# Performance work log

Hardware: AMD Instinct MI355X
Metric: run time of the kernel (lower is better)

## Reference

```python
import jax, jax.numpy as jnp
import numpy as np

B, N, M, C1, C2, H = 16, 4096, 1024, 256, 512, 256
SE_C = max(1, int(H / 24.0))  # 10
BN_EPS = 1e-5

def _bn(x, g, b):
    # training-mode BatchNorm over (B, n) per channel; x: [B, C, n]
    mean = jnp.mean(x, axis=(0, 2), keepdims=True)
    var = jnp.mean((x - mean) ** 2, axis=(0, 2), keepdims=True)  # biased var (torch)
    return (x - mean) * jax.lax.rsqrt(var + BN_EPS) * g[None, :, None] + b[None, :, None]

def _swish(x):
    return x * jax.nn.sigmoid(x)

def setup_inputs() -> dict:
    key = jax.random.key(0)
    ks = jax.random.split(key, 12)
    d = {
        "unknown": jax.random.normal(ks[0], (B, N, 3), jnp.float32),
        "known": jax.random.normal(ks[1], (B, M, 3), jnp.float32),
        "unknow_feats": jax.random.normal(ks[2], (B, C1, N), jnp.float32),
        "known_feats": jax.random.normal(ks[3], (B, C2, M), jnp.float32),
        # conv1 (C1+C2 -> H), no bias (bn)
        "W1": jax.random.normal(ks[4], (H, C1 + C2), jnp.float32) * (1.0 / np.sqrt(C1 + C2)),
        "g1": jnp.ones((H,), jnp.float32),
        "b1": jnp.zeros((H,), jnp.float32),
        # SE block (1x1 convs with bias, no pooling in this impl)
        "se_rw": jax.random.normal(ks[5], (SE_C, H), jnp.float32) * (1.0 / np.sqrt(H)),
        "se_rb": jnp.zeros((SE_C,), jnp.float32),
        "se_ew": jax.random.normal(ks[6], (H, SE_C), jnp.float32) * (1.0 / np.sqrt(SE_C)),
        "se_eb": jnp.zeros((H,), jnp.float32),
        # conv2 (H -> H), no bias
        "W2": jax.random.normal(ks[7], (H, H), jnp.float32) * (1.0 / np.sqrt(H)),
        "g2": jnp.ones((H,), jnp.float32),
        "b2": jnp.zeros((H,), jnp.float32),
    }
    return d

def reference(unknown, known, unknow_feats, known_feats,
              W1, g1, b1, se_rw, se_rb, se_ew, se_eb, W2, g2, b2):
    # three_nn: squared distances of each unknown point to all known points
    d2 = jnp.sum((unknown[:, :, None, :] - known[:, None, :, :]) ** 2, axis=-1)  # [B,N,M]
    neg_d, idx = jax.lax.top_k(-d2, 3)  # 3 smallest
    dist = -neg_d                                       # [B,N,3]
    dist_recip = 1.0 / (dist + 1e-8)
    weight = dist_recip / jnp.sum(dist_recip, axis=2, keepdims=True)  # [B,N,3]
    # three_interpolate: gather known_feats at idx, inverse-distance weighted sum
    gathered = jnp.take_along_axis(known_feats[:, :, None, :], idx[:, None, :, :], axis=3)  # [B,C2,N,3]
    interp = jnp.sum(gathered * weight[:, None, :, :], axis=-1)  # [B,C2,N]
    x = jnp.concatenate([interp, unknow_feats], axis=1)  # [B,C1+C2,N]
    # conv1 (1x1) + BN + SE
    h = jnp.einsum('oc,bcn->bon', W1, x)
    h = _bn(h, g1, b1)
    s = jnp.einsum('oc,bcn->bon', se_rw, h) + se_rb[None, :, None]
    s = _swish(s)
    s = jnp.einsum('oc,bcn->bon', se_ew, s) + se_eb[None, :, None]
    h = jax.nn.sigmoid(s) * h
    # conv2 (1x1) + BN + ReLU
    h = jnp.einsum('oc,bcn->bon', W2, h)
    h = _bn(h, g2, b2)
    return jax.nn.relu(h)  # [B, H, N]
```

## Files before the change

kernel.cpp:

```cpp
#include <hip/hip_runtime.h>
#include <math.h>

#define B_ 16
#define N_ 4096
#define M_ 1024
#define C1_ 256
#define C2_ 512
#define H_ 256
#define SEC_ 10
#define OC_ 8
#define BN_EPS 1e-5f

typedef _Float16 f16;
typedef f16 f16x8 __attribute__((ext_vector_type(8)));
typedef f16 f16x4 __attribute__((ext_vector_type(4)));
typedef f16 f16x2 __attribute__((ext_vector_type(2)));
typedef float f32x4 __attribute__((ext_vector_type(4)));

__global__ __launch_bounds__(256)
void three_nn_kernel(const float* __restrict__ unknown, const float* __restrict__ known,
                     int* __restrict__ idxp, float* __restrict__ wgtp)
{
    __shared__ float kx[M_], ky[M_], kz[M_];
    __shared__ float cd[4][64][3];
    __shared__ int   ci[4][64][3];
    const int b  = blockIdx.y;
    const int bn = blockIdx.x * 64;
    const int t  = threadIdx.x;
    const float* kb = known + (long)b * M_ * 3;

    {
        const float4 q0 = *(const float4*)(kb + 12*t);
        const float4 q1 = *(const float4*)(kb + 12*t + 4);
        const float4 q2 = *(const float4*)(kb + 12*t + 8);
        const int m = 4*t;
        kx[m+0]=q0.x; ky[m+0]=q0.y; kz[m+0]=q0.z;
        kx[m+1]=q0.w; ky[m+1]=q1.x; kz[m+1]=q1.y;
        kx[m+2]=q1.z; ky[m+2]=q1.w; kz[m+2]=q2.x;
        kx[m+3]=q2.y; ky[m+3]=q2.z; kz[m+3]=q2.w;
    }
    __syncthreads();

    const int w = t >> 6, ln = t & 63;
    const int n = bn + ln;
    const float* up = unknown + ((long)b * N_ + n) * 3;
    const float ux = up[0], uy = up[1], uz = up[2];

    float b0 = 1e30f, b1v = 1e30f, b2v = 1e30f;
    int j0 = 0, j1 = 0, j2 = 0;

    const int m0 = w * 256;
    for (int m = m0; m < m0 + 256; m += 4) {
        const float4 X = *(const float4*)&kx[m];
        const float4 Y = *(const float4*)&ky[m];
        const float4 Z = *(const float4*)&kz[m];
        const float px[4] = {X.x, X.y, X.z, X.w};
        const float py[4] = {Y.x, Y.y, Y.z, Y.w};
        const float pz[4] = {Z.x, Z.y, Z.z, Z.w};
        #pragma unroll
        for (int q = 0; q < 4; q++) {
            const float dx = ux - px[q], dy = uy - py[q], dz = uz - pz[q];
            const float d = dx*dx + dy*dy + dz*dz;
            if (d < b2v) {
                const int mm = m + q;
                if (d < b1v) {
                    b2v = b1v; j2 = j1;
                    if (d < b0) { b1v = b0; j1 = j0; b0 = d; j0 = mm; }
                    else        { b1v = d;  j1 = mm; }
                } else { b2v = d; j2 = mm; }
            }
        }
    }
    cd[w][ln][0] = b0;  cd[w][ln][1] = b1v; cd[w][ln][2] = b2v;
    ci[w][ln][0] = j0;  ci[w][ln][1] = j1;  ci[w][ln][2] = j2;
    __syncthreads();

    if (t < 64) {
        float d0 = cd[0][t][0], d1 = cd[0][t][1], d2 = cd[0][t][2];
        int   i0 = ci[0][t][0], i1 = ci[0][t][1], i2 = ci[0][t][2];
        #pragma unroll
        for (int c = 1; c < 4; c++) {
            #pragma unroll
            for (int j = 0; j < 3; j++) {
                const float d = cd[c][t][j];
                const int  ix = ci[c][t][j];
                if (d < d2) {
                    if (d < d1) {
                        d2 = d1; i2 = i1;
                        if (d < d0) { d1 = d0; i1 = i0; d0 = d; i0 = ix; }
                        else        { d1 = d;  i1 = ix; }
                    } else { d2 = d; i2 = ix; }
                }
            }
        }
        const float r0 = 1.f/(d0 + 1e-8f), r1 = 1.f/(d1 + 1e-8f), r2 = 1.f/(d2 + 1e-8f);
        const float rs = 1.f/(r0 + r1 + r2);
        const long base = ((long)b * N_ + bn + t) * 3;
        idxp[base+0] = i0; idxp[base+1] = i1; idxp[base+2] = i2;
        wgtp[base+0] = r0*rs; wgtp[base+1] = r1*rs; wgtp[base+2] = r2*rs;
    }
}

template<int MODE>
__global__ __launch_bounds__(256)
void gemm_mfma(const float* __restrict__ A, int lda,
               const float* __restrict__ Bf, const f16* __restrict__ Bh,
               long strideB, int ldb, int K,
               f16* __restrict__ Ch, long strideC, int ldc,
               const f16* __restrict__ Gt,
               const int* __restrict__ idxp, const float* __restrict__ wgtp,
               float* __restrict__ psum,
               const float* __restrict__ spart, const float* __restrict__ rbAdj,
               const float* __restrict__ se_ewp, const float* __restrict__ se_ebp,
               const float* __restrict__ a1p, const float* __restrict__ c1p)
{
    __shared__ __align__(16) f16 As[256*72];
    __shared__ __align__(16) f16 Bs[64*72];
    __shared__ float sswl[SEC_*64];

    const int b   = blockIdx.z;
    const int bn  = blockIdx.x * 64;
    const int tid = threadIdx.x;
    const int l = tid & 63, w = tid >> 6;
    const int lane16 = l & 15, quad = l >> 4;

    const float* Bfb = nullptr;
    const f16*   Bhb = nullptr;
    if constexpr (MODE == 2) Bhb = Bh + (long)b*strideB;
    else                     Bfb = Bf + (long)b*strideB;

    if constexpr (MODE == 2) {
        for (int i = tid; i < SEC_*64; i += 256) {
            const int j = i >> 6, nn = i & 63;
            float v = rbAdj[j];
            #pragma unroll
            for (int oc = 0; oc < OC_; oc++)
                v += spart[(((long)oc*B_ + b)*SEC_ + j)*N_ + bn + nn];
            sswl[j*64 + nn] = v / (1.f + __expf(-v));
        }
        __syncthreads();
    }

    f32x4 acc[4][4];
    #pragma unroll
    for (int i = 0; i < 4; i++)
        #pragma unroll
        for (int j = 0; j < 4; j++)
            acc[i][j] = (f32x4){0.f, 0.f, 0.f, 0.f};

    const int akb = (tid & 3) * 16;
    const int arw = tid >> 2;

    for (int k0 = 0; k0 < K; k0 += 64) {
        #pragma unroll
        for (int p = 0; p < 4; p++) {
            const int r = p*64 + arw;
            const float* src = A + (long)r*lda + k0 + akb;
            const float4 v0 = *(const float4*)(src);
            const float4 v1 = *(const float4*)(src + 4);
            const float4 v2 = *(const float4*)(src + 8);
            const float4 v3 = *(const float4*)(src + 12);
            f16x8 h0, h1;
            h0[0]=(f16)v0.x; h0[1]=(f16)v0.y; h0[2]=(f16)v0.z; h0[3]=(f16)v0.w;
            h0[4]=(f16)v1.x; h0[5]=(f16)v1.y; h0[6]=(f16)v1.z; h0[7]=(f16)v1.w;
            h1[0]=(f16)v2.x; h1[1]=(f16)v2.y; h1[2]=(f16)v2.z; h1[3]=(f16)v2.w;
            h1[4]=(f16)v3.x; h1[5]=(f16)v3.y; h1[6]=(f16)v3.z; h1[7]=(f16)v3.w;
            *(f16x8*)&As[r*72 + akb]     = h0;
            *(f16x8*)&As[r*72 + akb + 8] = h1;
        }
        #pragma unroll
        for (int it = 0; it < 2; it++) {
            const int slot = it*256 + tid;
            const int k2 = slot >> 4;
            const int n0 = (slot & 15) * 4;
            if constexpr (MODE == 2) {
                const int ka = k0 + 2*k2;
                const f16* s0 = Bhb + (long)ka*ldb + bn + n0;
                const f16x4 ua = *(const f16x4*)s0;
                const f16x4 ub = *(const f16x4*)(s0 + ldb);
                float val[2][4];
                #pragma unroll
                for (int r = 0; r < 2; r++) {
                    const int kr = ka + r;
                    const float aa = a1p[kr], cc = c1p[kr], eb = se_ebp[kr];
                    const float* ew = se_ewp + kr*SEC_;
                    #pragma unroll
                    for (int j = 0; j < 4; j++) {
                        float e = eb;
                        #pragma unroll
                        for (int q = 0; q < SEC_; q++) e += ew[q]*sswl[q*64 + n0 + j];
                        const float g  = 1.f/(1.f + __expf(-e));
                        const float hv = (r == 0) ? (float)ua[j] : (float)ub[j];
                        val[r][j] = g * (aa*hv + cc);
                    }
                }
                #pragma unroll
                for (int j = 0; j < 4; j++) {
                    f16x2 p; p[0] = (f16)val[0][j]; p[1] = (f16)val[1][j];
                    *(f16x2*)&Bs[(n0+j)*72 + 2*k2] = p;
                }
            } else {
                const float* s0 = Bfb + (long)(k0 + 2*k2)*ldb + bn + n0;
                const float4 u = *(const float4*)s0;
                const float4 v = *(const float4*)(s0 + ldb);
                f16x2 p0, p1, p2, p3;
                p0[0]=(f16)u.x; p0[1]=(f16)v.x;
                p1[0]=(f16)u.y; p1[1]=(f16)v.y;
                p2[0]=(f16)u.z; p2[1]=(f16)v.z;
                p3[0]=(f16)u.w; p3[1]=(f16)v.w;
                *(f16x2*)&Bs[(n0+0)*72 + 2*k2] = p0;
                *(f16x2*)&Bs[(n0+1)*72 + 2*k2] = p1;
                *(f16x2*)&Bs[(n0+2)*72 + 2*k2] = p2;
                *(f16x2*)&Bs[(n0+3)*72 + 2*k2] = p3;
            }
        }
        __syncthreads();
        const int abase = (w*64 + lane16)*72 + quad*8;
        const int bbase = lane16*72 + quad*8;
        #pragma unroll
        for (int s = 0; s < 2; s++) {
            f16x8 af[4], bf[4];
            #pragma unroll
            for (int i = 0; i < 4; i++) af[i] = *(const f16x8*)&As[abase + i*1152 + s*32];
            #pragma unroll
            for (int j = 0; j < 4; j++) bf[j] = *(const f16x8*)&Bs[bbase + j*1152 + s*32];
            #pragma unroll
            for (int i = 0; i < 4; i++)
                #pragma unroll
                for (int j = 0; j < 4; j++)
                    acc[i][j] = __builtin_amdgcn_mfma_f32_16x16x32_f16(af[i], bf[j], acc[i][j], 0, 0, 0);
        }
        __syncthreads();
    }

    if constexpr (MODE == 0) {
        f16* Gl = As;
        #pragma unroll
        for (int i = 0; i < 4; i++)
            #pragma unroll
            for (int r = 0; r < 4; r++) {
                const int h = w*64 + i*16 + quad*4 + r;
                #pragma unroll
                for (int j = 0; j < 4; j++)
                    Gl[(j*16 + lane16)*264 + h] = (f16)acc[i][j][r];
            }
        __syncthreads();
        f16* Gtb = Ch + (long)b*strideC + (long)bn*H_;
        #pragma unroll
        for (int it = 0; it < 8; it++) {
            const int t = it*256 + tid;
            const int m = t >> 5, c = (t & 31)*8;
            *(f16x8*)&Gtb[m*H_ + c] = *(const f16x8*)&Gl[m*264 + c];
        }
    } else {
        if constexpr (MODE == 1) {
            f16* P = As;
            const int p  = tid >> 2;
            const int qd = tid & 3;
            const long ib = ((long)b*N_ + bn + p)*3;
            const int i0 = idxp[ib], i1 = idxp[ib+1], i2 = idxp[ib+2];
            const float w0 = wgtp[ib], w1 = wgtp[ib+1], w2 = wgtp[ib+2];
            const f16* gb = Gt + (long)b*M_*H_;
            const f16* g0 = gb + (long)i0*H_ + qd*64;
            const f16* g1 = gb + (long)i1*H_ + qd*64;
            const f16* g2 = gb + (long)i2*H_ + qd*64;
            f16* Pr = P + p*264 + qd*64;
            #pragma unroll
            for (int c = 0; c < 64; c += 8) {
                const f16x8 x0 = *(const f16x8*)&g0[c];
                const f16x8 x1 = *(const f16x8*)&g1[c];
                const f16x8 x2 = *(const f16x8*)&g2[c];
                f16x8 o;
                #pragma unroll
                for (int e = 0; e < 8; e++)
                    o[e] = (f16)(w0*(float)x0[e] + w1*(float)x1[e] + w2*(float)x2[e]);
                *(f16x8*)&Pr[c] = o;
            }
            __syncthreads();
            #pragma unroll
            for (int i = 0; i < 4; i++)
                #pragma unroll
                for (int r = 0; r < 4; r++) {
                    const int h = w*64 + i*16 + quad*4 + r;
                    #pragma unroll
                    for (int j = 0; j < 4; j++)
                        acc[i][j][r] += (float)P[(j*16 + lane16)*264 + h];
                }
        }
        const int bid = blockIdx.z * gridDim.x + blockIdx.x;
        float* ps = psum + (long)bid * (2*H_);
        f16* Cb = Ch + (long)b*strideC;
        #pragma unroll
        for (int i = 0; i < 4; i++)
            #pragma unroll
            for (int r = 0; r < 4; r++) {
                const int row = w*64 + i*16 + quad*4 + r;
                float s1 = 0.f, s2 = 0.f;
                #pragma unroll
                for (int j = 0; j < 4; j++) {
                    const float v = acc[i][j][r];
                    s1 += v; s2 += v*v;
                    Cb[(long)row*ldc + bn + j*16 + lane16] = (f16)v;
                }
                #pragma unroll
                for (int off = 1; off < 16; off <<= 1) {
                    s1 += __shfl_xor(s1, off, 64);
                    s2 += __shfl_xor(s2, off, 64);
                }
                if (lane16 == 0) {
                    ps[row]      = s1;
                    ps[H_ + row] = s2;
                }
            }
    }
}

__global__ __launch_bounds__(256)
void reduce_stats_kernel(const float* __restrict__ psum, float* __restrict__ stats, int nblk)
{
    __shared__ float red[8][33];
    const int o  = blockIdx.x*32 + (threadIdx.x & 31);
    const int ch = threadIdx.x >> 5;
    float s = 0.f;
    for (int bid = ch; bid < nblk; bid += 8)
        s += psum[(long)bid*(2*H_) + o];
    red[ch][threadIdx.x & 31] = s;
    __syncthreads();
    if (ch == 0) {
        float t = 0.f;
        #pragma unroll
        for (int c = 0; c < 8; c++) t += red[c][threadIdx.x & 31];
        stats[o] = t;
    }
}

__global__ __launch_bounds__(256)
void finalize1_kernel(const float* __restrict__ stats,
                      const float* __restrict__ g, const float* __restrict__ bb,
                      const float* __restrict__ se_rw, const float* __restrict__ se_rb,
                      float* __restrict__ a1, float* __restrict__ c1,
                      float* __restrict__ rw2, float* __restrict__ rbAdj)
{
    __shared__ float cbuf[H_];
    __shared__ float red[256];
    const int o = threadIdx.x;
    const float inv = 1.f / (float)(B_ * N_);
    const float S1 = stats[o], S2 = stats[H_ + o];
    const float mean = S1 * inv;
    const float var  = S2 * inv - mean*mean;
    const float a = g[o] * rsqrtf(var + BN_EPS);
    const float c = bb[o] - mean*a;
    a1[o] = a; c1[o] = c; cbuf[o] = c;
    for (int j = 0; j < SEC_; j++) rw2[j*H_ + o] = se_rw[j*H_ + o] * a;
    __syncthreads();
    for (int j = 0; j < SEC_; j++) {
        red[o] = se_rw[j*H_ + o] * cbuf[o];
        __syncthreads();
        for (int s = 128; s > 0; s >>= 1) {
            if (o < s) red[o] += red[o + s];
            __syncthreads();
        }
        if (o == 0) rbAdj[j] = se_rb[j] + red[0];
        __syncthreads();
    }
}

__global__ __launch_bounds__(256)
void se_reduce_kernel(const f16* __restrict__ h1h, const float* __restrict__ rw2,
                      float* __restrict__ spart)
{
    constexpr int OCH = H_ / OC_;
    __shared__ float rwl[SEC_][OCH];
    const int b = blockIdx.y, oc = blockIdx.z;
    const int n0 = blockIdx.x*1024 + threadIdx.x*4;
    for (int i = threadIdx.x; i < SEC_*OCH; i += 256)
        rwl[i/OCH][i%OCH] = rw2[(i/OCH)*H_ + oc*OCH + (i%OCH)];
    __syncthreads();
    f32x4 acc[SEC_];
    #pragma unroll
    for (int j = 0; j < SEC_; j++) acc[j] = (f32x4){0.f,0.f,0.f,0.f};
    const f16* hp = h1h + ((long)b*H_ + oc*OCH)*N_ + n0;
    for (int o = 0; o < OCH; o++) {
        const f16x4 h = *(const f16x4*)(hp + (long)o*N_);
        f32x4 hf; hf[0]=(float)h[0]; hf[1]=(float)h[1]; hf[2]=(float)h[2]; hf[3]=(float)h[3];
        #pragma unroll
        for (int j = 0; j < SEC_; j++) acc[j] += rwl[j][o]*hf;
    }
    #pragma unroll
    for (int j = 0; j < SEC_; j++)
        *(f32x4*)&spart[(((long)oc*B_ + b)*SEC_ + j)*N_ + n0] = acc[j];
}

__global__ __launch_bounds__(256)
void finalize2_kernel(const float* __restrict__ stats,
                      const float* __restrict__ g, const float* __restrict__ bb,
                      float* __restrict__ a2, float* __restrict__ c2)
{
    const int o = threadIdx.x;
    const float inv = 1.f / (float)(B_ * N_);
    const float S1 = stats[o], S2 = stats[H_ + o];
    const float mean = S1 * inv;
    const float var  = S2 * inv - mean*mean;
    const float a = g[o] * rsqrtf(var + BN_EPS);
    a2[o] = a; c2[o] = bb[o] - mean*a;
}

__global__ __launch_bounds__(256)
void bn_relu_kernel(const f16* __restrict__ h2h, float* __restrict__ out,
                    const float* __restrict__ a2, const float* __restrict__ c2)
{
    const long e = ((long)blockIdx.x*256 + threadIdx.x)*8;
    const int o = (int)((e >> 12) & (H_ - 1));
    const f16x8 v = *(const f16x8*)(h2h + e);
    const float a = a2[o], c = c2[o];
    float4 r0, r1;
    r0.x = fmaxf(a*(float)v[0] + c, 0.f);
    r0.y = fmaxf(a*(float)v[1] + c, 0.f);
    r0.z = fmaxf(a*(float)v[2] + c, 0.f);
    r0.w = fmaxf(a*(float)v[3] + c, 0.f);
    r1.x = fmaxf(a*(float)v[4] + c, 0.f);
    r1.y = fmaxf(a*(float)v[5] + c, 0.f);
    r1.z = fmaxf(a*(float)v[6] + c, 0.f);
    r1.w = fmaxf(a*(float)v[7] + c, 0.f);
    *(float4*)(out + e)     = r0;
    *(float4*)(out + e + 4) = r1;
}

extern "C" void kernel_launch(void* const* d_in, const int* in_sizes, int n_in,
                              void* d_out, int out_size, void* d_ws, size_t ws_size,
                              hipStream_t stream)
{
    const float* unknown = (const float*)d_in[0];
    const float* known   = (const float*)d_in[1];
    const float* uf      = (const float*)d_in[2];
    const float* kf      = (const float*)d_in[3];
    const float* W1      = (const float*)d_in[4];
    const float* g1      = (const float*)d_in[5];
    const float* b1      = (const float*)d_in[6];
    const float* se_rw   = (const float*)d_in[7];
    const float* se_rb   = (const float*)d_in[8];
    const float* se_ew   = (const float*)d_in[9];
    const float* se_eb   = (const float*)d_in[10];
    const float* W2      = (const float*)d_in[11];
    const float* g2      = (const float*)d_in[12];
    const float* b2      = (const float*)d_in[13];

    char* ws = (char*)d_ws;
    size_t off = 0;
    auto alloc = [&](size_t bytes) -> void* {
        void* p = ws + off;
        off += (bytes + 255) & ~(size_t)255;
        return p;
    };
    const int NBLK = (N_/64) * B_;
    int*   idxp   = (int*)  alloc((size_t)B_*N_*3*4);
    float* wgtp   = (float*)alloc((size_t)B_*N_*3*4);
    f16*   Gt     = (f16*)  alloc((size_t)B_*M_*H_*2);
    f16*   h1h    = (f16*)  alloc((size_t)B_*H_*N_*2);
    f16*   h2h    = (f16*)  alloc((size_t)B_*H_*N_*2);
    float* spart  = (float*)alloc((size_t)OC_*B_*SEC_*N_*4);
    float* psum1  = (float*)alloc((size_t)NBLK*2*H_*4);
    float* psum2  = (float*)alloc((size_t)NBLK*2*H_*4);
    float* stats1 = (float*)alloc(2*H_*4);
    float* stats2 = (float*)alloc(2*H_*4);
    float* a1     = (float*)alloc(H_*4);
    float* c1     = (float*)alloc(H_*4);
    float* rw2    = (float*)alloc(SEC_*H_*4);
    float* rbAdj  = (float*)alloc(64*4);
    float* a2     = (float*)alloc(H_*4);
    float* c2     = (float*)alloc(H_*4);
    (void)ws_size; (void)in_sizes; (void)n_in; (void)out_size;

    float* out = (float*)d_out;

    three_nn_kernel<<<dim3(N_/64, B_), 256, 0, stream>>>(unknown, known, idxp, wgtp);

    gemm_mfma<0><<<dim3(M_/64, 1, B_), 256, 0, stream>>>(
        W1, C1_+C2_, kf, nullptr, (long)C2_*M_, M_, C2_,
        Gt, (long)M_*H_, 0,
        nullptr, nullptr, nullptr, nullptr,
        nullptr, nullptr, nullptr, nullptr, nullptr, nullptr);

    gemm_mfma<1><<<dim3(N_/64, 1, B_), 256, 0, stream>>>(
        W1 + C2_, C1_+C2_, uf, nullptr, (long)C1_*N_, N_, C1_,
        h1h, (long)H_*N_, N_,
        Gt, idxp, wgtp, psum1,
        nullptr, nullptr, nullptr, nullptr, nullptr, nullptr);

    reduce_stats_kernel<<<dim3(16), 256, 0, stream>>>(psum1, stats1, NBLK);

    finalize1_kernel<<<1, 256, 0, stream>>>(stats1, g1, b1, se_rw, se_rb, a1, c1, rw2, rbAdj);

    se_reduce_kernel<<<dim3(N_/1024, B_, OC_), 256, 0, stream>>>(h1h, rw2, spart);

    gemm_mfma<2><<<dim3(N_/64, 1, B_), 256, 0, stream>>>(
        W2, H_, nullptr, h1h, (long)H_*N_, N_, H_,
        h2h, (long)H_*N_, N_,
        nullptr, nullptr, nullptr, psum2,
        spart, rbAdj, se_ew, se_eb, a1, c1);

    reduce_stats_kernel<<<dim3(16), 256, 0, stream>>>(psum2, stats2, NBLK);

    finalize2_kernel<<<1, 256, 0, stream>>>(stats2, g2, b2, a2, c2);

    bn_relu_kernel<<<dim3((unsigned)((long)B_*H_*N_/2048)), 256, 0, stream>>>(h2h, out, a2, c2);
}
```

Measured before the change: 447.1 us.

## Pre-convert weights to fp16 fragment layout and double-buffer B tiles

A new kernel converts W1 and W2 to fp16 once per call and stores them in MFMA fragment order. The GEMMs then load A fragments straight from global memory (L2-cached) instead of converting fp32 weights and staging them through LDS on every block. B staging is double-buffered with a single barrier per k-step, so loads for the next tile overlap the MFMAs on the current one. The cost is an extra small launch plus direct global loads for A inside the inner loop, whose latency may not be hidden.

```diff
diff --git a/kernel.cpp b/kernel.cpp
--- a/kernel.cpp
+++ b/kernel.cpp
@@ -101,11 +101,36 @@
     }
 }
 
+__global__ __launch_bounds__(256)
+void convert_w_kernel(const float* __restrict__ W1, const float* __restrict__ W2,
+                      f16* __restrict__ Wf0, f16* __restrict__ Wf1, f16* __restrict__ Wf2)
+{
+    const int which = blockIdx.y;
+    const int K8    = (which == 0) ? 64 : 32;
+    const int lda   = (which == 2) ? 256 : 768;
+    const float* src = (which == 0) ? W1 : (which == 1) ? (W1 + 512) : W2;
+    f16* dst = (which == 0) ? Wf0 : (which == 1) ? Wf1 : Wf2;
+    const int t = blockIdx.x * 256 + threadIdx.x;
+    const int total = 16 * K8 * 16;
+    if (t >= total) return;
+    const int l16 = t & 15;
+    const int fi  = t >> 4;
+    const int k8  = fi & (K8 - 1);
+    const int rb  = fi >> ((which == 0) ? 6 : 5);
+    const float* s = src + (long)(rb*16 + l16)*lda + k8*8;
+    const float4 a = *(const float4*)s;
+    const float4 c = *(const float4*)(s + 4);
+    f16x8 h;
+    h[0]=(f16)a.x; h[1]=(f16)a.y; h[2]=(f16)a.z; h[3]=(f16)a.w;
+    h[4]=(f16)c.x; h[5]=(f16)c.y; h[6]=(f16)c.z; h[7]=(f16)c.w;
+    *(f16x8*)&dst[(long)t*8] = h;
+}
+
 template<int MODE>
 __global__ __launch_bounds__(256)
-void gemm_mfma(const float* __restrict__ A, int lda,
+void gemm_mfma(const f16* __restrict__ Af, int K,
                const float* __restrict__ Bf, const f16* __restrict__ Bh,
-               long strideB, int ldb, int K,
+               long strideB, int ldb,
                f16* __restrict__ Ch, long strideC, int ldc,
                const f16* __restrict__ Gt,
                const int* __restrict__ idxp, const float* __restrict__ wgtp,
@@ -114,15 +139,17 @@
                const float* __restrict__ se_ewp, const float* __restrict__ se_ebp,
                const float* __restrict__ a1p, const float* __restrict__ c1p)
 {
-    __shared__ __align__(16) f16 As[256*72];
-    __shared__ __align__(16) f16 Bs[64*72];
+    __shared__ __align__(16) char smem[64*264*2];
     __shared__ float sswl[SEC_*64];
+    f16* const BsA = (f16*)smem;
+    f16* const BsB = (f16*)(smem + 64*72*2);
 
     const int b   = blockIdx.z;
     const int bn  = blockIdx.x * 64;
     const int tid = threadIdx.x;
     const int l = tid & 63, w = tid >> 6;
     const int lane16 = l & 15, quad = l >> 4;
+    const int K8 = K >> 3;
 
     const float* Bfb = nullptr;
     const f16*   Bhb = nullptr;
@@ -148,26 +175,7 @@
         for (int j = 0; j < 4; j++)
             acc[i][j] = (f32x4){0.f, 0.f, 0.f, 0.f};
 
-    const int akb = (tid & 3) * 16;
-    const int arw = tid >> 2;
-
-    for (int k0 = 0; k0 < K; k0 += 64) {
-        #pragma unroll
-        for (int p = 0; p < 4; p++) {
-            const int r = p*64 + arw;
-            const float* src = A + (long)r*lda + k0 + akb;
-            const float4 v0 = *(const float4*)(src);
-            const float4 v1 = *(const float4*)(src + 4);
-            const float4 v2 = *(const float4*)(src + 8);
-            const float4 v3 = *(const float4*)(src + 12);
-            f16x8 h0, h1;
-            h0[0]=(f16)v0.x; h0[1]=(f16)v0.y; h0[2]=(f16)v0.z; h0[3]=(f16)v0.w;
-            h0[4]=(f16)v1.x; h0[5]=(f16)v1.y; h0[6]=(f16)v1.z; h0[7]=(f16)v1.w;
-            h1[0]=(f16)v2.x; h1[1]=(f16)v2.y; h1[2]=(f16)v2.z; h1[3]=(f16)v2.w;
-            h1[4]=(f16)v3.x; h1[5]=(f16)v3.y; h1[6]=(f16)v3.z; h1[7]=(f16)v3.w;
-            *(f16x8*)&As[r*72 + akb]     = h0;
-            *(f16x8*)&As[r*72 + akb + 8] = h1;
-        }
+    auto stageB = [&](int k0, f16* __restrict__ Bsb) {
         #pragma unroll
         for (int it = 0; it < 2; it++) {
             const int slot = it*256 + tid;
@@ -197,7 +205,7 @@
                 #pragma unroll
                 for (int j = 0; j < 4; j++) {
                     f16x2 p; p[0] = (f16)val[0][j]; p[1] = (f16)val[1][j];
-                    *(f16x2*)&Bs[(n0+j)*72 + 2*k2] = p;
+                    *(f16x2*)&Bsb[(n0+j)*72 + 2*k2] = p;
                 }
             } else {
                 const float* s0 = Bfb + (long)(k0 + 2*k2)*ldb + bn + n0;
@@ -208,22 +216,35 @@
                 p1[0]=(f16)u.y; p1[1]=(f16)v.y;
                 p2[0]=(f16)u.z; p2[1]=(f16)v.z;
                 p3[0]=(f16)u.w; p3[1]=(f16)v.w;
-                *(f16x2*)&Bs[(n0+0)*72 + 2*k2] = p0;
-                *(f16x2*)&Bs[(n0+1)*72 + 2*k2] = p1;
-                *(f16x2*)&Bs[(n0+2)*72 + 2*k2] = p2;
-                *(f16x2*)&Bs[(n0+3)*72 + 2*k2] = p3;
+                *(f16x2*)&Bsb[(n0+0)*72 + 2*k2] = p0;
+                *(f16x2*)&Bsb[(n0+1)*72 + 2*k2] = p1;
+                *(f16x2*)&Bsb[(n0+2)*72 + 2*k2] = p2;
+                *(f16x2*)&Bsb[(n0+3)*72 + 2*k2] = p3;
             }
         }
-        __syncthreads();
-        const int abase = (w*64 + lane16)*72 + quad*8;
-        const int bbase = lane16*72 + quad*8;
+    };
+
+    const f16* Afp = Af + quad*128 + lane16*8;
+    const int bbase = lane16*72 + quad*8;
+
+    stageB(0, BsA);
+    __syncthreads();
+
+    const int NKT = K >> 6;
+    int cur = 0;
+    for (int kt = 0; kt < NKT; kt++) {
+        f16* const Bcur = cur ? BsB : BsA;
+        if (kt + 1 < NKT) stageB((kt+1) << 6, cur ? BsA : BsB);
         #pragma unroll
         for (int s = 0; s < 2; s++) {
+            const int ks = kt*2 + s;
             f16x8 af[4], bf[4];
             #pragma unroll
-            for (int i = 0; i < 4; i++) af[i] = *(const f16x8*)&As[abase + i*1152 + s*32];
-            #pragma unroll
-            for (int j = 0; j < 4; j++) bf[j] = *(const f16x8*)&Bs[bbase + j*1152 + s*32];
+            for (int i = 0; i < 4; i++)
+                af[i] = *(const f16x8*)(Afp + (long)((w*4 + i)*K8 + ks*4)*128);
+            #pragma unroll
+            for (int j = 0; j < 4; j++)
+                bf[j] = *(const f16x8*)&Bcur[bbase + j*1152 + s*32];
             #pragma unroll
             for (int i = 0; i < 4; i++)
                 #pragma unroll
@@ -231,10 +252,11 @@
                     acc[i][j] = __builtin_amdgcn_mfma_f32_16x16x32_f16(af[i], bf[j], acc[i][j], 0, 0, 0);
         }
         __syncthreads();
+        cur ^= 1;
     }
 
     if constexpr (MODE == 0) {
-        f16* Gl = As;
+        f16* Gl = (f16*)smem;
         #pragma unroll
         for (int i = 0; i < 4; i++)
             #pragma unroll
@@ -254,7 +276,7 @@
         }
     } else {
         if constexpr (MODE == 1) {
-            f16* P = As;
+            f16* P = (f16*)smem;
             const int p  = tid >> 2;
             const int qd = tid & 3;
             const long ib = ((long)b*N_ + bn + p)*3;
@@ -277,6 +299,7 @@
                 *(f16x8*)&Pr[c] = o;
             }
             __syncthreads();
+            f16* P2 = (f16*)smem;
             #pragma unroll
             for (int i = 0; i < 4; i++)
                 #pragma unroll
@@ -284,7 +307,7 @@
                     const int h = w*64 + i*16 + quad*4 + r;
                     #pragma unroll
                     for (int j = 0; j < 4; j++)
-                        acc[i][j][r] += (float)P[(j*16 + lane16)*264 + h];
+                        acc[i][j][r] += (float)P2[(j*16 + lane16)*264 + h];
                 }
         }
         const int bid = blockIdx.z * gridDim.x + blockIdx.x;
@@ -469,20 +492,25 @@
     float* rbAdj  = (float*)alloc(64*4);
     float* a2     = (float*)alloc(H_*4);
     float* c2     = (float*)alloc(H_*4);
+    f16*   Wf0    = (f16*)  alloc((size_t)H_*C2_*2);
+    f16*   Wf1    = (f16*)  alloc((size_t)H_*C1_*2);
+    f16*   Wf2    = (f16*)  alloc((size_t)H_*H_*2);
     (void)ws_size; (void)in_sizes; (void)n_in; (void)out_size;
 
     float* out = (float*)d_out;
 
+    convert_w_kernel<<<dim3(64, 3), 256, 0, stream>>>(W1, W2, Wf0, Wf1, Wf2);
+
     three_nn_kernel<<<dim3(N_/64, B_), 256, 0, stream>>>(unknown, known, idxp, wgtp);
 
     gemm_mfma<0><<<dim3(M_/64, 1, B_), 256, 0, stream>>>(
-        W1, C1_+C2_, kf, nullptr, (long)C2_*M_, M_, C2_,
+        Wf0, C2_, kf, nullptr, (long)C2_*M_, M_,
         Gt, (long)M_*H_, 0,
         nullptr, nullptr, nullptr, nullptr,
         nullptr, nullptr, nullptr, nullptr, nullptr, nullptr);
 
     gemm_mfma<1><<<dim3(N_/64, 1, B_), 256, 0, stream>>>(
-        W1 + C2_, C1_+C2_, uf, nullptr, (long)C1_*N_, N_, C1_,
+        Wf1, C1_, uf, nullptr, (long)C1_*N_, N_,
         h1h, (long)H_*N_, N_,
         Gt, idxp, wgtp, psum1,
         nullptr, nullptr, nullptr, nullptr, nullptr, nullptr);
@@ -494,7 +522,7 @@
     se_reduce_kernel<<<dim3(N_/1024, B_, OC_), 256, 0, stream>>>(h1h, rw2, spart);
 
     gemm_mfma<2><<<dim3(N_/64, 1, B_), 256, 0, stream>>>(
-        W2, H_, nullptr, h1h, (long)H_*N_, N_, H_,
+        Wf2, H_, nullptr, h1h, (long)H_*N_, N_,
         h2h, (long)H_*N_, N_,
         nullptr, nullptr, nullptr, psum2,
         spart, rbAdj, se_ew, se_eb, a1, c1);
```

New measurement: 408.4 us. 1.09x faster.
